# Performance work log

Hardware: AMD Instinct MI355X
Metric: run time of the kernel (lower is better)

The kernel has to match this reference:

```python
import jax, jax.numpy as jnp
import numpy as np

B, T, C, H = 65536, 100, 7, 2  # batch, timesteps, covariates, lstm hidden


def setup_inputs() -> dict:
    key = jax.random.key(0)
    ks = iter(jax.random.split(key, 32))
    def rn(shape, s=0.1):
        return jax.random.normal(next(ks), shape, dtype=jnp.float32) * s
    inp = {"x": jax.random.normal(next(ks), (B, T, C), dtype=jnp.float32)}
    for l, din in ((0, C), (1, 2 * H)):
        for suf in ("", "r"):
            inp[f"w_ih_l{l}{suf}"] = rn((4 * H, din))
            inp[f"w_hh_l{l}{suf}"] = rn((4 * H, H))
            inp[f"b_ih_l{l}{suf}"] = rn((4 * H,))
            inp[f"b_hh_l{l}{suf}"] = rn((4 * H,))
    inp["fc1_w"] = rn((64, 4 * T))
    inp["fc1_b"] = rn((64,))
    inp["fc2_w"] = rn((20, 64))
    inp["fc2_b"] = rn((20,))
    return inp


def _lstm_dir(xw, w_hh, b_hh, reverse):
    # xw: [T, B, 4H] precomputed input projection (x @ W_ih.T + b_ih)
    if reverse:
        xw = xw[::-1]
    h0 = jnp.zeros((xw.shape[1], H), xw.dtype)
    c0 = jnp.zeros((xw.shape[1], H), xw.dtype)

    def step(carry, gx):
        h, c = carry
        g = gx + h @ w_hh.T + b_hh            # [B, 4H]
        i, f, gg, o = jnp.split(g, 4, axis=-1)  # torch gate order i,f,g,o
        c = jax.nn.sigmoid(f) * c + jax.nn.sigmoid(i) * jnp.tanh(gg)
        h = jax.nn.sigmoid(o) * jnp.tanh(c)
        return (h, c), h

    _, hs = jax.lax.scan(step, (h0, c0), xw)
    if reverse:
        hs = hs[::-1]
    return hs  # [T, B, H]


def _bilstm_layer(x_tbf, w_ih_f, w_hh_f, b_ih_f, b_hh_f,
                  w_ih_b, w_hh_b, b_ih_b, b_hh_b):
    xw_f = jnp.einsum('tbc,gc->tbg', x_tbf, w_ih_f) + b_ih_f
    xw_b = jnp.einsum('tbc,gc->tbg', x_tbf, w_ih_b) + b_ih_b
    hf = _lstm_dir(xw_f, w_hh_f, b_hh_f, False)
    hb = _lstm_dir(xw_b, w_hh_b, b_hh_b, True)
    return jnp.concatenate([hf, hb], axis=-1)  # [T, B, 2H]


def reference(x,
              w_ih_l0, w_hh_l0, b_ih_l0, b_hh_l0,
              w_ih_l0r, w_hh_l0r, b_ih_l0r, b_hh_l0r,
              w_ih_l1, w_hh_l1, b_ih_l1, b_hh_l1,
              w_ih_l1r, w_hh_l1r, b_ih_l1r, b_hh_l1r,
              fc1_w, fc1_b, fc2_w, fc2_b):
    xt = jnp.transpose(x.reshape(-1, T, C), (1, 0, 2))  # [T, B, C] time-major
    h1 = _bilstm_layer(xt, w_ih_l0, w_hh_l0, b_ih_l0, b_hh_l0,
                       w_ih_l0r, w_hh_l0r, b_ih_l0r, b_hh_l0r)
    h2 = _bilstm_layer(h1, w_ih_l1, w_hh_l1, b_ih_l1, b_hh_l1,
                       w_ih_l1r, w_hh_l1r, b_ih_l1r, b_hh_l1r)
    out = jnp.transpose(h2, (1, 0, 2)).reshape(-1, 4 * T)  # flatten [B, 4T]
    out = jax.nn.relu(out)                  # relu BEFORE fc1, as in original
    out = jax.nn.relu(out @ fc1_w.T + fc1_b)
    return out @ fc2_w.T + fc2_b            # [B, 20]
```

## Files before the change

kernel.cpp:

```cpp
#include <hip/hip_runtime.h>

#define Bn 65536
#define Tn 100
#define Cn 7

typedef short short8 __attribute__((ext_vector_type(8)));
typedef float float4v __attribute__((ext_vector_type(4)));
typedef float float2v __attribute__((ext_vector_type(2)));

__device__ __forceinline__ float2v pk_fma(float2v a, float2v b, float2v c) {
    return __builtin_elementwise_fma(a, b, c);
}
__device__ __forceinline__ float2v pk2(float v) { return (float2v){v, v}; }

__device__ __forceinline__ float fast_rcp(float x) { return __builtin_amdgcn_rcpf(x); }
__device__ __forceinline__ float sig_f(float x) { return fast_rcp(1.f + __expf(-x)); }
__device__ __forceinline__ float tanh_f(float x) { return 1.f - 2.f * fast_rcp(__expf(2.f * x) + 1.f); }
__device__ __forceinline__ unsigned bf16rne(float x) {
    unsigned u = __float_as_uint(x);
    return (u + 0x7fffu + ((u >> 16) & 1u)) >> 16;
}
__device__ __forceinline__ float bf_lo(unsigned u) { return __uint_as_float(u << 16); }
__device__ __forceinline__ float bf_hi(unsigned u) { return __uint_as_float(u & 0xffff0000u); }

__device__ __forceinline__ float dpp_xor1(float x) {
    return __uint_as_float((unsigned)__builtin_amdgcn_mov_dpp(
        (int)__float_as_uint(x), 0xB1, 0xF, 0xF, true));
}

typedef const __attribute__((address_space(1))) void* gp_t;
typedef __attribute__((address_space(3))) void* sp_t;
__device__ __forceinline__ void async_copy_dw(const void* g, void* l) {
    __builtin_amdgcn_global_load_lds((gp_t)g, (sp_t)l, 4, 0, 0);
}

__global__ void w2prep_kernel(const float* __restrict__ fc1_w, unsigned short* __restrict__ w2g) {
    int idx = blockIdx.x * 256 + threadIdx.x;
    int w  = idx >> 12;
    int d  = (idx >> 11) & 1;
    int n  = (idx >> 5) & 63;
    int kk = idx & 31;
    int tt = kk >> 1, i = kk & 1;
    int t  = d ? (99 - 10 * w - tt) : (10 * w + tt);
    float v = (kk < 20) ? fc1_w[n * 400 + 4 * t + 2 * d + i] : 0.f;
    w2g[idx] = (unsigned short)bf16rne(v);
}

#define XFE(i) (xv[(i) >> 2][(i) & 3])
#define L0_STEP(RR, TV) do {                                                          \
    float2v g0 = bias2[0], g1 = bias2[1];                                             \
    g0 = pk_fma(wi2[0][0], pk2(XFE((RR)*7+0)), g0);                                   \
    g1 = pk_fma(wi2[1][0], pk2(XFE((RR)*7+0)), g1);                                   \
    g0 = pk_fma(wi2[0][1], pk2(XFE((RR)*7+1)), g0);                                   \
    g1 = pk_fma(wi2[1][1], pk2(XFE((RR)*7+1)), g1);                                   \
    g0 = pk_fma(wi2[0][2], pk2(XFE((RR)*7+2)), g0);                                   \
    g1 = pk_fma(wi2[1][2], pk2(XFE((RR)*7+2)), g1);                                   \
    g0 = pk_fma(wi2[0][3], pk2(XFE((RR)*7+3)), g0);                                   \
    g1 = pk_fma(wi2[1][3], pk2(XFE((RR)*7+3)), g1);                                   \
    g0 = pk_fma(wi2[0][4], pk2(XFE((RR)*7+4)), g0);                                   \
    g1 = pk_fma(wi2[1][4], pk2(XFE((RR)*7+4)), g1);                                   \
    g0 = pk_fma(wi2[0][5], pk2(XFE((RR)*7+5)), g0);                                   \
    g1 = pk_fma(wi2[1][5], pk2(XFE((RR)*7+5)), g1);                                   \
    g0 = pk_fma(wi2[0][6], pk2(XFE((RR)*7+6)), g0);                                   \
    g1 = pk_fma(wi2[1][6], pk2(XFE((RR)*7+6)), g1);                                   \
    g0 = pk_fma(whA2[0], pk2(hs), pk_fma(whB2[0], pk2(ho), g0));                      \
    g1 = pk_fma(whA2[1], pk2(hs), pk_fma(whB2[1], pk2(ho), g1));                      \
    const float iv = sig_f(g0.x);                                                     \
    const float fv = sig_f(g0.y);                                                     \
    const float qv = tanh_f(g1.x);                                                    \
    const float ov = sig_f(g1.y);                                                     \
    cc = fmaf(fv, cc, iv * qv);                                                       \
    hs = ov * tanh_f(cc);                                                             \
    ho = dpp_xor1(hs);                                                                \
    if (cid == 0)                                                                     \
        h1u[((size_t)(TV) * 2 + rev) * Bn + b] = bf16rne(hs) | (bf16rne(ho) << 16);   \
} while (0)

__global__ __launch_bounds__(256, 4) void l0_kernel(
    const float* __restrict__ x,
    const float* __restrict__ wih_f, const float* __restrict__ whh_f,
    const float* __restrict__ bih_f, const float* __restrict__ bhh_f,
    const float* __restrict__ wih_r, const float* __restrict__ whh_r,
    const float* __restrict__ bih_r, const float* __restrict__ bhh_r,
    unsigned* __restrict__ h1u)
{
    __shared__ float xs[4][2][896];

    const int tid  = threadIdx.x;
    const int wv   = tid >> 6;
    const int lane = tid & 63;
    const int rev  = wv >> 1;
    const int sgrp = wv & 1;
    const int cid  = lane & 1;
    const int s    = lane >> 1;
    const int b    = blockIdx.x * 64 + sgrp * 32 + s;

    const float* wih = rev ? wih_r : wih_f;
    const float* whh = rev ? whh_r : whh_f;
    const float* bih = rev ? bih_r : bih_f;
    const float* bhh = rev ? bhh_r : bhh_f;

    float2v wi2[2][7], whA2[2], whB2[2], bias2[2];
#pragma unroll
    for (int p = 0; p < 2; ++p) {
        const int k0 = cid + 4 * p, k1 = cid + 4 * p + 2;
#pragma unroll
        for (int c = 0; c < 7; ++c)
            wi2[p][c] = (float2v){wih[k0 * 7 + c], wih[k1 * 7 + c]};
        whA2[p]  = (float2v){whh[k0 * 2 + cid], whh[k1 * 2 + cid]};
        whB2[p]  = (float2v){whh[k0 * 2 + (cid ^ 1)], whh[k1 * 2 + (cid ^ 1)]};
        bias2[p] = (float2v){bih[k0] + bhh[k0], bih[k1] + bhh[k1]};
    }

    const int s0 = lane / 28;
    const int r0 = lane - 28 * s0;
    const float* xsamp = x + (size_t)(blockIdx.x * 64 + sgrp * 32 + s0) * 700;

    auto stage = [&](int ch, int p) {
        const int off = rev ? (672 - 28 * ch) : (28 * ch);
        const float* g = xsamp + off + r0;
        float* l = &xs[wv][p][lane];
        int r = r0;
#pragma unroll
        for (int i = 0; i < 14; ++i) {
            async_copy_dw(g, l);
            l += 64;
            const int c = (r >= 20) ? 1 : 0;
            g += c ? 2080 : 1408;
            r += c ? -20 : 8;
        }
    };

    float hs = 0.f, ho = 0.f, cc = 0.f;

    stage(0, 0);
#pragma unroll 1
    for (int chk = 0; chk < 25; ++chk) {
        if (chk == 0) __builtin_amdgcn_s_waitcnt(0x0F70);
        else          __builtin_amdgcn_s_waitcnt(0x0F74);
        __builtin_amdgcn_sched_barrier(0);
        if (chk < 24) stage(chk + 1, (chk + 1) & 1);
        __builtin_amdgcn_sched_barrier(0);

        const float* xp = &xs[wv][chk & 1][s * 28];
        float4v xv[7];
#pragma unroll
        for (int k = 0; k < 7; ++k) xv[k] = *(const float4v*)(xp + k * 4);

        if (rev) {
            const int t0 = 99 - 4 * chk;
            L0_STEP(3, t0);
            L0_STEP(2, t0 - 1);
            L0_STEP(1, t0 - 2);
            L0_STEP(0, t0 - 3);
        } else {
            const int t0 = 4 * chk;
            L0_STEP(0, t0);
            L0_STEP(1, t0 + 1);
            L0_STEP(2, t0 + 2);
            L0_STEP(3, t0 + 3);
        }
    }
}

__global__ __launch_bounds__(256, 4) void l1fc_kernel(
    const unsigned* __restrict__ hin,
    const float* __restrict__ wih_f, const float* __restrict__ whh_f,
    const float* __restrict__ bih_f, const float* __restrict__ bhh_f,
    const float* __restrict__ wih_r, const float* __restrict__ whh_r,
    const float* __restrict__ bih_r, const float* __restrict__ bhh_r,
    const unsigned* __restrict__ w2g,
    const float* __restrict__ fc1_b,
    const float* __restrict__ fc2_w,
    const float* __restrict__ fc2_b,
    float* __restrict__ out)
{
    __shared__ unsigned smem[7680];

    const int tid  = threadIdx.x;
    const int wv   = tid >> 6;
    const int lane = tid & 63;
    const int d    = wv >> 1;
    const int shalf = wv & 1;
    const int cid  = lane & 1;
    const int sp   = lane >> 1;
    const int b0   = blockIdx.x * 64;

    unsigned* a2w  = smem + wv * 640;
    unsigned* hstw = smem + 2560 + wv * 1280;

    const float* wih = d ? wih_r : wih_f;
    const float* whh = d ? whh_r : whh_f;
    const float* bih = d ? bih_r : bih_f;
    const float* bhh = d ? bhh_r : bhh_f;

    float2v wi2[2][4], whA2[2], whB2[2], bias2[2];
#pragma unroll
    for (int p = 0; p < 2; ++p) {
        const int k0 = cid + 4 * p, k1 = cid + 4 * p + 2;
#pragma unroll
        for (int m = 0; m < 4; ++m)
            wi2[p][m] = (float2v){wih[k0 * 4 + m], wih[k1 * 4 + m]};
        whA2[p]  = (float2v){whh[k0 * 2 + cid], whh[k1 * 2 + cid]};
        whB2[p]  = (float2v){whh[k0 * 2 + (cid ^ 1)], whh[k1 * 2 + (cid ^ 1)]};
        bias2[p] = (float2v){bih[k0] + bhh[k0], bih[k1] + bhh[k1]};
    }

    float4v acc[2][4];
#pragma unroll
    for (int mt = 0; mt < 2; ++mt)
#pragma unroll
        for (int nt = 0; nt < 4; ++nt) acc[mt][nt] = (float4v){0.f, 0.f, 0.f, 0.f};

    for (int i = lane; i < 640; i += 64) a2w[i] = 0u;

    auto stage_h = [&](int w, int pb) {
        unsigned* dst = hstw + pb * 640;
        const int col = lane & 31;
        const int Rb  = lane >> 5;
#pragma unroll
        for (int i = 0; i < 10; ++i) {
            const int R = Rb + 2 * i;
            const int p = (R >= 10) ? 1 : 0;
            const int j = R - 10 * p;
            const int t = d ? (99 - (10 * w + j)) : (10 * w + j);
            async_copy_dw(hin + ((size_t)t * 2 + p) * Bn + b0 + shalf * 32 + col,
                          dst + R * 32 + col);
        }
    };

    stage_h(0, 0);

    float hs = 0.f, ho = 0.f, cc = 0.f;
    const int q = lane >> 4, l16 = lane & 15;

#pragma unroll 1
    for (int w = 0; w < 10; ++w) {
        __builtin_amdgcn_s_waitcnt(0x0F70);
        __builtin_amdgcn_sched_barrier(0);

        short8 bv[4];
#pragma unroll
        for (int nt = 0; nt < 4; ++nt)
            bv[nt] = *(const short8*)&w2g[w * 2048 + d * 1024 + (nt * 16 + l16) * 16 + q * 4];

        if (w < 9) stage_h(w + 1, (w + 1) & 1);
        __builtin_amdgcn_sched_barrier(0);

        const unsigned* hb = hstw + (w & 1) * 640;
#pragma unroll 2
        for (int j = 0; j < 10; ++j) {
            const unsigned uF = hb[j * 32 + sp];
            const unsigned uR = hb[320 + j * 32 + sp];
            const float a0 = bf_lo(uF), a1 = bf_hi(uF);
            const float a2v = bf_lo(uR), a3 = bf_hi(uR);

            float2v g0 = bias2[0], g1 = bias2[1];
            g0 = pk_fma(wi2[0][0], pk2(a0), g0);  g1 = pk_fma(wi2[1][0], pk2(a0), g1);
            g0 = pk_fma(wi2[0][1], pk2(a1), g0);  g1 = pk_fma(wi2[1][1], pk2(a1), g1);
            g0 = pk_fma(wi2[0][2], pk2(a2v), g0); g1 = pk_fma(wi2[1][2], pk2(a2v), g1);
            g0 = pk_fma(wi2[0][3], pk2(a3), g0);  g1 = pk_fma(wi2[1][3], pk2(a3), g1);
            g0 = pk_fma(whA2[0], pk2(hs), pk_fma(whB2[0], pk2(ho), g0));
            g1 = pk_fma(whA2[1], pk2(hs), pk_fma(whB2[1], pk2(ho), g1));

            const float iv = sig_f(g0.x);
            const float fv = sig_f(g0.y);
            const float qv = tanh_f(g1.x);
            const float ov = sig_f(g1.y);
            cc = fmaf(fv, cc, iv * qv);
            hs = ov * tanh_f(cc);
            ho = dpp_xor1(hs);

            if (cid == 0)
                a2w[sp * 20 + j] = bf16rne(fmaxf(hs, 0.f)) | (bf16rne(fmaxf(ho, 0.f)) << 16);
        }
        asm volatile("s_waitcnt lgkmcnt(0)");
        __builtin_amdgcn_sched_barrier(0);

        {
            short8 av0 = *(const short8*)&a2w[l16 * 20 + q * 4];
            short8 av1 = *(const short8*)&a2w[(16 + l16) * 20 + q * 4];
#pragma unroll
            for (int nt = 0; nt < 4; ++nt) {
                acc[0][nt] = __builtin_amdgcn_mfma_f32_16x16x32_bf16(av0, bv[nt], acc[0][nt], 0, 0, 0);
                acc[1][nt] = __builtin_amdgcn_mfma_f32_16x16x32_bf16(av1, bv[nt], acc[1][nt], 0, 0, 0);
            }
        }
    }

    __syncthreads();
    float* eb = (float*)smem;
    if (d == 0) {
#pragma unroll
        for (int mt = 0; mt < 2; ++mt)
#pragma unroll
            for (int nt = 0; nt < 4; ++nt)
#pragma unroll
                for (int r = 0; r < 4; ++r)
                    eb[(shalf * 32 + mt * 16 + q * 4 + r) * 65 + nt * 16 + l16] = acc[mt][nt][r];
    }
    __syncthreads();
    if (d == 1) {
#pragma unroll
        for (int mt = 0; mt < 2; ++mt)
#pragma unroll
            for (int nt = 0; nt < 4; ++nt)
#pragma unroll
                for (int r = 0; r < 4; ++r)
                    eb[(shalf * 32 + mt * 16 + q * 4 + r) * 65 + nt * 16 + l16] += acc[mt][nt][r];
    }
    __syncthreads();

    const float* ebr = (const float*)smem;
    const int sm2 = tid & 63;
    const int og  = (tid >> 6) * 5;
    float z[64];
#pragma unroll
    for (int k = 0; k < 64; ++k) z[k] = fmaxf(ebr[sm2 * 65 + k] + fc1_b[k], 0.f);
    float y[5];
#pragma unroll
    for (int o = 0; o < 5; ++o) {
        float r2 = fc2_b[og + o];
#pragma unroll
        for (int k = 0; k < 64; ++k) r2 = fmaf(fc2_w[(og + o) * 64 + k], z[k], r2);
        y[o] = r2;
    }
    __syncthreads();
    float* ebw = (float*)smem;
#pragma unroll
    for (int o = 0; o < 5; ++o) ebw[sm2 * 20 + og + o] = y[o];
    __syncthreads();
    for (int f = tid; f < 1280; f += 256)
        out[(size_t)blockIdx.x * 1280 + f] = ebw[f];
}

extern "C" void kernel_launch(void* const* d_in, const int* in_sizes, int n_in,
                              void* d_out, int out_size, void* d_ws, size_t ws_size,
                              hipStream_t stream) {
    const float* x = (const float*)d_in[0];
    const float* w_ih_l0  = (const float*)d_in[1];
    const float* w_hh_l0  = (const float*)d_in[2];
    const float* b_ih_l0  = (const float*)d_in[3];
    const float* b_hh_l0  = (const float*)d_in[4];
    const float* w_ih_l0r = (const float*)d_in[5];
    const float* w_hh_l0r = (const float*)d_in[6];
    const float* b_ih_l0r = (const float*)d_in[7];
    const float* b_hh_l0r = (const float*)d_in[8];
    const float* w_ih_l1  = (const float*)d_in[9];
    const float* w_hh_l1  = (const float*)d_in[10];
    const float* b_ih_l1  = (const float*)d_in[11];
    const float* b_hh_l1  = (const float*)d_in[12];
    const float* w_ih_l1r = (const float*)d_in[13];
    const float* w_hh_l1r = (const float*)d_in[14];
    const float* b_ih_l1r = (const float*)d_in[15];
    const float* b_hh_l1r = (const float*)d_in[16];
    const float* fc1_w = (const float*)d_in[17];
    const float* fc1_b = (const float*)d_in[18];
    const float* fc2_w = (const float*)d_in[19];
    const float* fc2_b = (const float*)d_in[20];

    unsigned* h1u = (unsigned*)d_ws;
    unsigned short* w2g = (unsigned short*)((char*)d_ws + (size_t)Tn * 2 * Bn * 4);

    w2prep_kernel<<<160, 256, 0, stream>>>(fc1_w, w2g);
    l0_kernel<<<1024, 256, 0, stream>>>(x,
        w_ih_l0, w_hh_l0, b_ih_l0, b_hh_l0,
        w_ih_l0r, w_hh_l0r, b_ih_l0r, b_hh_l0r, h1u);
    l1fc_kernel<<<1024, 256, 0, stream>>>(h1u,
        w_ih_l1, w_hh_l1, b_ih_l1, b_hh_l1,
        w_ih_l1r, w_hh_l1r, b_ih_l1r, b_hh_l1r,
        (const unsigned*)w2g, fc1_b, fc2_w, fc2_b, (float*)d_out);
}
```

Measured before the change: 404.7 us.

## Split layer-0 LSTM gates across four lanes per sample instead of two

The layer-0 kernel now uses four lanes per (sample, direction) instead of two. Each lane computes one pair of gate pre-activations and one activation pair. Sigmoid and tanh share a single exp/rcp path selected by per-lane constants, and gates are exchanged with a DPP xor-2 swap. The grid doubles to 2048 blocks with 16 samples per wave, which halves the serial per-lane work on the recurrence's critical path. The cost is twice as many waves doing redundant x loads and cell-state updates, plus extra cross-lane moves.

```diff
diff --git a/kernel.cpp b/kernel.cpp
--- a/kernel.cpp
+++ b/kernel.cpp
@@ -26,6 +26,10 @@
 __device__ __forceinline__ float dpp_xor1(float x) {
     return __uint_as_float((unsigned)__builtin_amdgcn_mov_dpp(
         (int)__float_as_uint(x), 0xB1, 0xF, 0xF, true));
+}
+__device__ __forceinline__ float dpp_xor2(float x) {
+    return __uint_as_float((unsigned)__builtin_amdgcn_mov_dpp(
+        (int)__float_as_uint(x), 0x4E, 0xF, 0xF, true));
 }
 
 typedef const __attribute__((address_space(1))) void* gp_t;
@@ -48,32 +52,34 @@
 
 #define XFE(i) (xv[(i) >> 2][(i) & 3])
 #define L0_STEP(RR, TV) do {                                                          \
-    float2v g0 = bias2[0], g1 = bias2[1];                                             \
-    g0 = pk_fma(wi2[0][0], pk2(XFE((RR)*7+0)), g0);                                   \
-    g1 = pk_fma(wi2[1][0], pk2(XFE((RR)*7+0)), g1);                                   \
-    g0 = pk_fma(wi2[0][1], pk2(XFE((RR)*7+1)), g0);                                   \
-    g1 = pk_fma(wi2[1][1], pk2(XFE((RR)*7+1)), g1);                                   \
-    g0 = pk_fma(wi2[0][2], pk2(XFE((RR)*7+2)), g0);                                   \
-    g1 = pk_fma(wi2[1][2], pk2(XFE((RR)*7+2)), g1);                                   \
-    g0 = pk_fma(wi2[0][3], pk2(XFE((RR)*7+3)), g0);                                   \
-    g1 = pk_fma(wi2[1][3], pk2(XFE((RR)*7+3)), g1);                                   \
-    g0 = pk_fma(wi2[0][4], pk2(XFE((RR)*7+4)), g0);                                   \
-    g1 = pk_fma(wi2[1][4], pk2(XFE((RR)*7+4)), g1);                                   \
-    g0 = pk_fma(wi2[0][5], pk2(XFE((RR)*7+5)), g0);                                   \
-    g1 = pk_fma(wi2[1][5], pk2(XFE((RR)*7+5)), g1);                                   \
-    g0 = pk_fma(wi2[0][6], pk2(XFE((RR)*7+6)), g0);                                   \
-    g1 = pk_fma(wi2[1][6], pk2(XFE((RR)*7+6)), g1);                                   \
-    g0 = pk_fma(whA2[0], pk2(hs), pk_fma(whB2[0], pk2(ho), g0));                      \
-    g1 = pk_fma(whA2[1], pk2(hs), pk_fma(whB2[1], pk2(ho), g1));                      \
-    const float iv = sig_f(g0.x);                                                     \
-    const float fv = sig_f(g0.y);                                                     \
-    const float qv = tanh_f(g1.x);                                                    \
-    const float ov = sig_f(g1.y);                                                     \
-    cc = fmaf(fv, cc, iv * qv);                                                       \
-    hs = ov * tanh_f(cc);                                                             \
-    ho = dpp_xor1(hs);                                                                \
-    if (cid == 0)                                                                     \
-        h1u[((size_t)(TV) * 2 + rev) * Bn + b] = bf16rne(hs) | (bf16rne(ho) << 16);   \
+    float2v g = bias2;                                                                \
+    g = pk_fma(wi2[0], pk2(XFE((RR)*7+0)), g);                                        \
+    g = pk_fma(wi2[1], pk2(XFE((RR)*7+1)), g);                                        \
+    g = pk_fma(wi2[2], pk2(XFE((RR)*7+2)), g);                                        \
+    g = pk_fma(wi2[3], pk2(XFE((RR)*7+3)), g);                                        \
+    g = pk_fma(wi2[4], pk2(XFE((RR)*7+4)), g);                                        \
+    g = pk_fma(wi2[5], pk2(XFE((RR)*7+5)), g);                                        \
+    g = pk_fma(wi2[6], pk2(XFE((RR)*7+6)), g);                                        \
+    g = pk_fma(whX2, pk2(hA), pk_fma(whY2, pk2(hB), g));                              \
+    const float ex  = __expf(kx * g.x);                                               \
+    const float ey  = __expf(-g.y);                                                   \
+    const float rx  = fast_rcp(1.f + ex);                                             \
+    const float ry  = fast_rcp(1.f + ey);                                             \
+    const float acx = fmaf(ax_, rx, bx_);                                             \
+    const float acy = ry;                                                             \
+    const float swx = dpp_xor2(acx);                                                  \
+    const float swy = dpp_xor2(acy);                                                  \
+    const float iv  = qif ? acx : swx;                                                \
+    const float fv  = qif ? acy : swy;                                                \
+    const float gv  = qif ? swx : acx;                                                \
+    const float ov  = qif ? swy : acy;                                                \
+    cc = fmaf(fv, cc, iv * gv);                                                       \
+    const float th = tanh_f(cc);                                                      \
+    const float h  = ov * th;                                                         \
+    hB = dpp_xor1(h);                                                                 \
+    hA = h;                                                                           \
+    if (q == 0)                                                                       \
+        h1u[((size_t)(TV) * 2 + rev) * Bn + b] = bf16rne(hA) | (bf16rne(hB) << 16);   \
 } while (0)
 
 __global__ __launch_bounds__(256, 4) void l0_kernel(
@@ -84,45 +90,50 @@
     const float* __restrict__ bih_r, const float* __restrict__ bhh_r,
     unsigned* __restrict__ h1u)
 {
-    __shared__ float xs[4][2][896];
+    __shared__ float xs[4][2][448];
 
     const int tid  = threadIdx.x;
     const int wv   = tid >> 6;
     const int lane = tid & 63;
     const int rev  = wv >> 1;
     const int sgrp = wv & 1;
-    const int cid  = lane & 1;
-    const int s    = lane >> 1;
-    const int b    = blockIdx.x * 64 + sgrp * 32 + s;
+    const int sq   = lane >> 2;
+    const int q    = lane & 3;
+    const int ch   = q & 1;
+    const bool qif = (q & 2) == 0;
+    const int b    = blockIdx.x * 32 + sgrp * 16 + sq;
 
     const float* wih = rev ? wih_r : wih_f;
     const float* whh = rev ? whh_r : whh_f;
     const float* bih = rev ? bih_r : bih_f;
     const float* bhh = rev ? bhh_r : bhh_f;
 
-    float2v wi2[2][7], whA2[2], whB2[2], bias2[2];
-#pragma unroll
-    for (int p = 0; p < 2; ++p) {
-        const int k0 = cid + 4 * p, k1 = cid + 4 * p + 2;
-#pragma unroll
-        for (int c = 0; c < 7; ++c)
-            wi2[p][c] = (float2v){wih[k0 * 7 + c], wih[k1 * 7 + c]};
-        whA2[p]  = (float2v){whh[k0 * 2 + cid], whh[k1 * 2 + cid]};
-        whB2[p]  = (float2v){whh[k0 * 2 + (cid ^ 1)], whh[k1 * 2 + (cid ^ 1)]};
-        bias2[p] = (float2v){bih[k0] + bhh[k0], bih[k1] + bhh[k1]};
-    }
+    const int r0_ = (qif ? 0 : 4) + ch;
+    const int r1_ = (qif ? 2 : 6) + ch;
+
+    float2v wi2[7], whX2, whY2, bias2;
+#pragma unroll
+    for (int c = 0; c < 7; ++c)
+        wi2[c] = (float2v){wih[r0_ * 7 + c], wih[r1_ * 7 + c]};
+    whX2  = (float2v){whh[r0_ * 2 + ch], whh[r1_ * 2 + ch]};
+    whY2  = (float2v){whh[r0_ * 2 + (ch ^ 1)], whh[r1_ * 2 + (ch ^ 1)]};
+    bias2 = (float2v){bih[r0_] + bhh[r0_], bih[r1_] + bhh[r1_]};
+
+    const float kx  = qif ? -1.f : 2.f;
+    const float ax_ = qif ?  1.f : -2.f;
+    const float bx_ = qif ?  0.f : 1.f;
 
     const int s0 = lane / 28;
     const int r0 = lane - 28 * s0;
-    const float* xsamp = x + (size_t)(blockIdx.x * 64 + sgrp * 32 + s0) * 700;
-
-    auto stage = [&](int ch, int p) {
-        const int off = rev ? (672 - 28 * ch) : (28 * ch);
+    const float* xsamp = x + (size_t)(blockIdx.x * 32 + sgrp * 16 + s0) * 700;
+
+    auto stage = [&](int ch_, int p) {
+        const int off = rev ? (672 - 28 * ch_) : (28 * ch_);
         const float* g = xsamp + off + r0;
         float* l = &xs[wv][p][lane];
         int r = r0;
 #pragma unroll
-        for (int i = 0; i < 14; ++i) {
+        for (int i = 0; i < 7; ++i) {
             async_copy_dw(g, l);
             l += 64;
             const int c = (r >= 20) ? 1 : 0;
@@ -131,7 +142,7 @@
         }
     };
 
-    float hs = 0.f, ho = 0.f, cc = 0.f;
+    float hA = 0.f, hB = 0.f, cc = 0.f;
 
     stage(0, 0);
 #pragma unroll 1
@@ -142,7 +153,7 @@
         if (chk < 24) stage(chk + 1, (chk + 1) & 1);
         __builtin_amdgcn_sched_barrier(0);
 
-        const float* xp = &xs[wv][chk & 1][s * 28];
+        const float* xp = &xs[wv][chk & 1][sq * 28];
         float4v xv[7];
 #pragma unroll
         for (int k = 0; k < 7; ++k) xv[k] = *(const float4v*)(xp + k * 4);
@@ -363,7 +374,7 @@
     unsigned short* w2g = (unsigned short*)((char*)d_ws + (size_t)Tn * 2 * Bn * 4);
 
     w2prep_kernel<<<160, 256, 0, stream>>>(fc1_w, w2g);
-    l0_kernel<<<1024, 256, 0, stream>>>(x,
+    l0_kernel<<<2048, 256, 0, stream>>>(x,
         w_ih_l0, w_hh_l0, b_ih_l0, b_hh_l0,
         w_ih_l0r, w_hh_l0r, b_ih_l0r, b_hh_l0r, h1u);
     l1fc_kernel<<<1024, 256, 0, stream>>>(h1u,
```

Result: no change. 408.2 us (+0.9%).

## Fuse layer-0 and layer-1 LSTM kernels per block and prescale gates for exp2

Applied to the files above, without the earlier changes.

Merges the layer-0 BiLSTM kernel and the layer-1+FC kernel into one kernel. Each block computes its own 64 samples through both layers, with a vmcnt wait and block barrier between the phases, so the second launch and its tail are removed and h1 is likely re-read from L2. Gate weights and biases are premultiplied by log2(e) (or 2*log2(e) for the tanh gate) so activations use raw v_exp_f32 without an extra multiply. Launch bounds rise from 4 to 5 waves per SIMD, which may tighten register allocation. The fused kernel's footprint is the larger of the two phases.

```diff
diff --git a/kernel.cpp b/kernel.cpp
--- a/kernel.cpp
+++ b/kernel.cpp
@@ -3,6 +3,8 @@
 #define Bn 65536
 #define Tn 100
 #define Cn 7
+#define LOG2E  1.4426950408889634f
+#define LOG2E2 2.8853900817779268f
 
 typedef short short8 __attribute__((ext_vector_type(8)));
 typedef float float4v __attribute__((ext_vector_type(4)));
@@ -14,8 +16,12 @@
 __device__ __forceinline__ float2v pk2(float v) { return (float2v){v, v}; }
 
 __device__ __forceinline__ float fast_rcp(float x) { return __builtin_amdgcn_rcpf(x); }
-__device__ __forceinline__ float sig_f(float x) { return fast_rcp(1.f + __expf(-x)); }
-__device__ __forceinline__ float tanh_f(float x) { return 1.f - 2.f * fast_rcp(__expf(2.f * x) + 1.f); }
+__device__ __forceinline__ float exp2_f(float x) {
+    float r; asm("v_exp_f32 %0, %1" : "=v"(r) : "v"(x)); return r;
+}
+__device__ __forceinline__ float tanh2_f(float x) {
+    return 1.f - 2.f * fast_rcp(exp2_f(LOG2E2 * x) + 1.f);
+}
 __device__ __forceinline__ unsigned bf16rne(float x) {
     unsigned u = __float_as_uint(x);
     return (u + 0x7fffu + ((u >> 16) & 1u)) >> 16;
@@ -65,110 +71,28 @@
     g1 = pk_fma(wi2[1][6], pk2(XFE((RR)*7+6)), g1);                                   \
     g0 = pk_fma(whA2[0], pk2(hs), pk_fma(whB2[0], pk2(ho), g0));                      \
     g1 = pk_fma(whA2[1], pk2(hs), pk_fma(whB2[1], pk2(ho), g1));                      \
-    const float iv = sig_f(g0.x);                                                     \
-    const float fv = sig_f(g0.y);                                                     \
-    const float qv = tanh_f(g1.x);                                                    \
-    const float ov = sig_f(g1.y);                                                     \
+    const float iv = fast_rcp(1.f + exp2_f(-g0.x));                                   \
+    const float fv = fast_rcp(1.f + exp2_f(-g0.y));                                   \
+    const float qv = 1.f - 2.f * fast_rcp(exp2_f(g1.x) + 1.f);                        \
+    const float ov = fast_rcp(1.f + exp2_f(-g1.y));                                   \
     cc = fmaf(fv, cc, iv * qv);                                                       \
-    hs = ov * tanh_f(cc);                                                             \
+    hs = ov * tanh2_f(cc);                                                            \
     ho = dpp_xor1(hs);                                                                \
     if (cid == 0)                                                                     \
         h1u[((size_t)(TV) * 2 + rev) * Bn + b] = bf16rne(hs) | (bf16rne(ho) << 16);   \
 } while (0)
 
-__global__ __launch_bounds__(256, 4) void l0_kernel(
+__global__ __launch_bounds__(256, 5) void fused_kernel(
     const float* __restrict__ x,
-    const float* __restrict__ wih_f, const float* __restrict__ whh_f,
-    const float* __restrict__ bih_f, const float* __restrict__ bhh_f,
-    const float* __restrict__ wih_r, const float* __restrict__ whh_r,
-    const float* __restrict__ bih_r, const float* __restrict__ bhh_r,
-    unsigned* __restrict__ h1u)
-{
-    __shared__ float xs[4][2][896];
-
-    const int tid  = threadIdx.x;
-    const int wv   = tid >> 6;
-    const int lane = tid & 63;
-    const int rev  = wv >> 1;
-    const int sgrp = wv & 1;
-    const int cid  = lane & 1;
-    const int s    = lane >> 1;
-    const int b    = blockIdx.x * 64 + sgrp * 32 + s;
-
-    const float* wih = rev ? wih_r : wih_f;
-    const float* whh = rev ? whh_r : whh_f;
-    const float* bih = rev ? bih_r : bih_f;
-    const float* bhh = rev ? bhh_r : bhh_f;
-
-    float2v wi2[2][7], whA2[2], whB2[2], bias2[2];
-#pragma unroll
-    for (int p = 0; p < 2; ++p) {
-        const int k0 = cid + 4 * p, k1 = cid + 4 * p + 2;
-#pragma unroll
-        for (int c = 0; c < 7; ++c)
-            wi2[p][c] = (float2v){wih[k0 * 7 + c], wih[k1 * 7 + c]};
-        whA2[p]  = (float2v){whh[k0 * 2 + cid], whh[k1 * 2 + cid]};
-        whB2[p]  = (float2v){whh[k0 * 2 + (cid ^ 1)], whh[k1 * 2 + (cid ^ 1)]};
-        bias2[p] = (float2v){bih[k0] + bhh[k0], bih[k1] + bhh[k1]};
-    }
-
-    const int s0 = lane / 28;
-    const int r0 = lane - 28 * s0;
-    const float* xsamp = x + (size_t)(blockIdx.x * 64 + sgrp * 32 + s0) * 700;
-
-    auto stage = [&](int ch, int p) {
-        const int off = rev ? (672 - 28 * ch) : (28 * ch);
-        const float* g = xsamp + off + r0;
-        float* l = &xs[wv][p][lane];
-        int r = r0;
-#pragma unroll
-        for (int i = 0; i < 14; ++i) {
-            async_copy_dw(g, l);
-            l += 64;
-            const int c = (r >= 20) ? 1 : 0;
-            g += c ? 2080 : 1408;
-            r += c ? -20 : 8;
-        }
-    };
-
-    float hs = 0.f, ho = 0.f, cc = 0.f;
-
-    stage(0, 0);
-#pragma unroll 1
-    for (int chk = 0; chk < 25; ++chk) {
-        if (chk == 0) __builtin_amdgcn_s_waitcnt(0x0F70);
-        else          __builtin_amdgcn_s_waitcnt(0x0F74);
-        __builtin_amdgcn_sched_barrier(0);
-        if (chk < 24) stage(chk + 1, (chk + 1) & 1);
-        __builtin_amdgcn_sched_barrier(0);
-
-        const float* xp = &xs[wv][chk & 1][s * 28];
-        float4v xv[7];
-#pragma unroll
-        for (int k = 0; k < 7; ++k) xv[k] = *(const float4v*)(xp + k * 4);
-
-        if (rev) {
-            const int t0 = 99 - 4 * chk;
-            L0_STEP(3, t0);
-            L0_STEP(2, t0 - 1);
-            L0_STEP(1, t0 - 2);
-            L0_STEP(0, t0 - 3);
-        } else {
-            const int t0 = 4 * chk;
-            L0_STEP(0, t0);
-            L0_STEP(1, t0 + 1);
-            L0_STEP(2, t0 + 2);
-            L0_STEP(3, t0 + 3);
-        }
-    }
-}
-
-__global__ __launch_bounds__(256, 4) void l1fc_kernel(
-    const unsigned* __restrict__ hin,
-    const float* __restrict__ wih_f, const float* __restrict__ whh_f,
-    const float* __restrict__ bih_f, const float* __restrict__ bhh_f,
-    const float* __restrict__ wih_r, const float* __restrict__ whh_r,
-    const float* __restrict__ bih_r, const float* __restrict__ bhh_r,
+    const float* __restrict__ wih0_f, const float* __restrict__ whh0_f,
+    const float* __restrict__ bih0_f, const float* __restrict__ bhh0_f,
+    const float* __restrict__ wih0_r, const float* __restrict__ whh0_r,
+    const float* __restrict__ bih0_r, const float* __restrict__ bhh0_r,
+    unsigned* __restrict__ h1u,
+    const float* __restrict__ wih1_f, const float* __restrict__ whh1_f,
+    const float* __restrict__ bih1_f, const float* __restrict__ bhh1_f,
+    const float* __restrict__ wih1_r, const float* __restrict__ whh1_r,
+    const float* __restrict__ bih1_r, const float* __restrict__ bhh1_r,
     const unsigned* __restrict__ w2g,
     const float* __restrict__ fc1_b,
     const float* __restrict__ fc2_w,
@@ -180,158 +104,243 @@
     const int tid  = threadIdx.x;
     const int wv   = tid >> 6;
     const int lane = tid & 63;
-    const int d    = wv >> 1;
-    const int shalf = wv & 1;
-    const int cid  = lane & 1;
-    const int sp   = lane >> 1;
-    const int b0   = blockIdx.x * 64;
-
-    unsigned* a2w  = smem + wv * 640;
-    unsigned* hstw = smem + 2560 + wv * 1280;
-
-    const float* wih = d ? wih_r : wih_f;
-    const float* whh = d ? whh_r : whh_f;
-    const float* bih = d ? bih_r : bih_f;
-    const float* bhh = d ? bhh_r : bhh_f;
-
-    float2v wi2[2][4], whA2[2], whB2[2], bias2[2];
-#pragma unroll
-    for (int p = 0; p < 2; ++p) {
-        const int k0 = cid + 4 * p, k1 = cid + 4 * p + 2;
-#pragma unroll
-        for (int m = 0; m < 4; ++m)
-            wi2[p][m] = (float2v){wih[k0 * 4 + m], wih[k1 * 4 + m]};
-        whA2[p]  = (float2v){whh[k0 * 2 + cid], whh[k1 * 2 + cid]};
-        whB2[p]  = (float2v){whh[k0 * 2 + (cid ^ 1)], whh[k1 * 2 + (cid ^ 1)]};
-        bias2[p] = (float2v){bih[k0] + bhh[k0], bih[k1] + bhh[k1]};
+
+    {
+        float* xs = (float*)smem;
+        const int rev  = wv >> 1;
+        const int sgrp = wv & 1;
+        const int cid  = lane & 1;
+        const int s    = lane >> 1;
+        const int b    = blockIdx.x * 64 + sgrp * 32 + s;
+
+        const float* wih = rev ? wih0_r : wih0_f;
+        const float* whh = rev ? whh0_r : whh0_f;
+        const float* bih = rev ? bih0_r : bih0_f;
+        const float* bhh = rev ? bhh0_r : bhh0_f;
+
+        const float2v sc[2] = { (float2v){LOG2E, LOG2E}, (float2v){LOG2E2, LOG2E} };
+        float2v wi2[2][7], whA2[2], whB2[2], bias2[2];
+#pragma unroll
+        for (int p = 0; p < 2; ++p) {
+            const int k0 = cid + 4 * p, k1 = cid + 4 * p + 2;
+#pragma unroll
+            for (int c = 0; c < 7; ++c)
+                wi2[p][c] = (float2v){wih[k0 * 7 + c], wih[k1 * 7 + c]} * sc[p];
+            whA2[p]  = (float2v){whh[k0 * 2 + cid], whh[k1 * 2 + cid]} * sc[p];
+            whB2[p]  = (float2v){whh[k0 * 2 + (cid ^ 1)], whh[k1 * 2 + (cid ^ 1)]} * sc[p];
+            bias2[p] = (float2v){bih[k0] + bhh[k0], bih[k1] + bhh[k1]} * sc[p];
+        }
+
+        const int s0 = lane / 28;
+        const int r0 = lane - 28 * s0;
+        const float* xsamp = x + (size_t)(blockIdx.x * 64 + sgrp * 32 + s0) * 700;
+
+        auto stage = [&](int ch, int p) {
+            const int off = rev ? (672 - 28 * ch) : (28 * ch);
+            const float* g = xsamp + off + r0;
+            float* l = xs + wv * 1792 + p * 896 + lane;
+            int r = r0;
+#pragma unroll
+            for (int i = 0; i < 14; ++i) {
+                async_copy_dw(g, l);
+                l += 64;
+                const int c = (r >= 20) ? 1 : 0;
+                g += c ? 2080 : 1408;
+                r += c ? -20 : 8;
+            }
+        };
+
+        float hs = 0.f, ho = 0.f, cc = 0.f;
+
+        stage(0, 0);
+#pragma unroll 1
+        for (int chk = 0; chk < 25; ++chk) {
+            if (chk == 0) __builtin_amdgcn_s_waitcnt(0x0F70);
+            else          __builtin_amdgcn_s_waitcnt(0x0F74);
+            __builtin_amdgcn_sched_barrier(0);
+            if (chk < 24) stage(chk + 1, (chk + 1) & 1);
+            __builtin_amdgcn_sched_barrier(0);
+
+            const float* xp = xs + wv * 1792 + (chk & 1) * 896 + s * 28;
+            float4v xv[7];
+#pragma unroll
+            for (int k = 0; k < 7; ++k) xv[k] = *(const float4v*)(xp + k * 4);
+
+            if (rev) {
+                const int t0 = 99 - 4 * chk;
+                L0_STEP(3, t0);
+                L0_STEP(2, t0 - 1);
+                L0_STEP(1, t0 - 2);
+                L0_STEP(0, t0 - 3);
+            } else {
+                const int t0 = 4 * chk;
+                L0_STEP(0, t0);
+                L0_STEP(1, t0 + 1);
+                L0_STEP(2, t0 + 2);
+                L0_STEP(3, t0 + 3);
+            }
+        }
     }
 
-    float4v acc[2][4];
-#pragma unroll
-    for (int mt = 0; mt < 2; ++mt)
-#pragma unroll
-        for (int nt = 0; nt < 4; ++nt) acc[mt][nt] = (float4v){0.f, 0.f, 0.f, 0.f};
-
-    for (int i = lane; i < 640; i += 64) a2w[i] = 0u;
-
-    auto stage_h = [&](int w, int pb) {
-        unsigned* dst = hstw + pb * 640;
-        const int col = lane & 31;
-        const int Rb  = lane >> 5;
-#pragma unroll
-        for (int i = 0; i < 10; ++i) {
-            const int R = Rb + 2 * i;
-            const int p = (R >= 10) ? 1 : 0;
-            const int j = R - 10 * p;
-            const int t = d ? (99 - (10 * w + j)) : (10 * w + j);
-            async_copy_dw(hin + ((size_t)t * 2 + p) * Bn + b0 + shalf * 32 + col,
-                          dst + R * 32 + col);
-        }
-    };
-
-    stage_h(0, 0);
-
-    float hs = 0.f, ho = 0.f, cc = 0.f;
-    const int q = lane >> 4, l16 = lane & 15;
+    asm volatile("s_waitcnt vmcnt(0)");
+    __syncthreads();
+
+    {
+        const unsigned* hin = (const unsigned*)h1u;
+        const int d     = wv >> 1;
+        const int shalf = wv & 1;
+        const int cid   = lane & 1;
+        const int sp    = lane >> 1;
+        const int b0    = blockIdx.x * 64;
+
+        unsigned* a2w  = smem + wv * 640;
+        unsigned* hstw = smem + 2560 + wv * 1280;
+
+        const float* wih = d ? wih1_r : wih1_f;
+        const float* whh = d ? whh1_r : whh1_f;
+        const float* bih = d ? bih1_r : bih1_f;
+        const float* bhh = d ? bhh1_r : bhh1_f;
+
+        const float2v sc[2] = { (float2v){LOG2E, LOG2E}, (float2v){LOG2E2, LOG2E} };
+        float2v wi2[2][4], whA2[2], whB2[2], bias2[2];
+#pragma unroll
+        for (int p = 0; p < 2; ++p) {
+            const int k0 = cid + 4 * p, k1 = cid + 4 * p + 2;
+#pragma unroll
+            for (int m = 0; m < 4; ++m)
+                wi2[p][m] = (float2v){wih[k0 * 4 + m], wih[k1 * 4 + m]} * sc[p];
+            whA2[p]  = (float2v){whh[k0 * 2 + cid], whh[k1 * 2 + cid]} * sc[p];
+            whB2[p]  = (float2v){whh[k0 * 2 + (cid ^ 1)], whh[k1 * 2 + (cid ^ 1)]} * sc[p];
+            bias2[p] = (float2v){bih[k0] + bhh[k0], bih[k1] + bhh[k1]} * sc[p];
+        }
+
+        float4v acc[2][4];
+#pragma unroll
+        for (int mt = 0; mt < 2; ++mt)
+#pragma unroll
+            for (int nt = 0; nt < 4; ++nt) acc[mt][nt] = (float4v){0.f, 0.f, 0.f, 0.f};
+
+        for (int i = lane; i < 640; i += 64) a2w[i] = 0u;
+
+        auto stage_h = [&](int w, int pb) {
+            unsigned* dst = hstw + pb * 640;
+            const int col = lane & 31;
+            const int Rb  = lane >> 5;
+#pragma unroll
+            for (int i = 0; i < 10; ++i) {
+                const int R = Rb + 2 * i;
+                const int p = (R >= 10) ? 1 : 0;
+                const int j = R - 10 * p;
+                const int t = d ? (99 - (10 * w + j)) : (10 * w + j);
+                async_copy_dw(hin + ((size_t)t * 2 + p) * Bn + b0 + shalf * 32 + col,
+                              dst + R * 32 + col);
+            }
+        };
+
+        stage_h(0, 0);
+
+        float hs = 0.f, ho = 0.f, cc = 0.f;
+        const int q = lane >> 4, l16 = lane & 15;
 
 #pragma unroll 1
-    for (int w = 0; w < 10; ++w) {
-        __builtin_amdgcn_s_waitcnt(0x0F70);
-        __builtin_amdgcn_sched_barrier(0);
-
-        short8 bv[4];
-#pragma unroll
-        for (int nt = 0; nt < 4; ++nt)
-            bv[nt] = *(const short8*)&w2g[w * 2048 + d * 1024 + (nt * 16 + l16) * 16 + q * 4];
-
-        if (w < 9) stage_h(w + 1, (w + 1) & 1);
-        __builtin_amdgcn_sched_barrier(0);
-
-        const unsigned* hb = hstw + (w & 1) * 640;
+        for (int w = 0; w < 10; ++w) {
+            __builtin_amdgcn_s_waitcnt(0x0F70);
+            __builtin_amdgcn_sched_barrier(0);
+
+            short8 bv[4];
+#pragma unroll
+            for (int nt = 0; nt < 4; ++nt)
+                bv[nt] = *(const short8*)&w2g[w * 2048 + d * 1024 + (nt * 16 + l16) * 16 + q * 4];
+
+            if (w < 9) stage_h(w + 1, (w + 1) & 1);
+            __builtin_amdgcn_sched_barrier(0);
+
+            const unsigned* hb = hstw + (w & 1) * 640;
 #pragma unroll 2
-        for (int j = 0; j < 10; ++j) {
-            const unsigned uF = hb[j * 32 + sp];
-            const unsigned uR = hb[320 + j * 32 + sp];
-            const float a0 = bf_lo(uF), a1 = bf_hi(uF);
-            const float a2v = bf_lo(uR), a3 = bf_hi(uR);
-
-            float2v g0 = bias2[0], g1 = bias2[1];
-            g0 = pk_fma(wi2[0][0], pk2(a0), g0);  g1 = pk_fma(wi2[1][0], pk2(a0), g1);
-            g0 = pk_fma(wi2[0][1], pk2(a1), g0);  g1 = pk_fma(wi2[1][1], pk2(a1), g1);
-            g0 = pk_fma(wi2[0][2], pk2(a2v), g0); g1 = pk_fma(wi2[1][2], pk2(a2v), g1);
-            g0 = pk_fma(wi2[0][3], pk2(a3), g0);  g1 = pk_fma(wi2[1][3], pk2(a3), g1);
-            g0 = pk_fma(whA2[0], pk2(hs), pk_fma(whB2[0], pk2(ho), g0));
-            g1 = pk_fma(whA2[1], pk2(hs), pk_fma(whB2[1], pk2(ho), g1));
-
-            const float iv = sig_f(g0.x);
-            const float fv = sig_f(g0.y);
-            const float qv = tanh_f(g1.x);
-            const float ov = sig_f(g1.y);
-            cc = fmaf(fv, cc, iv * qv);
-            hs = ov * tanh_f(cc);
-            ho = dpp_xor1(hs);
-
-            if (cid == 0)
-                a2w[sp * 20 + j] = bf16rne(fmaxf(hs, 0.f)) | (bf16rne(fmaxf(ho, 0.f)) << 16);
-        }
-        asm volatile("s_waitcnt lgkmcnt(0)");
-        __builtin_amdgcn_sched_barrier(0);
-
-        {
-            short8 av0 = *(const short8*)&a2w[l16 * 20 + q * 4];
-            short8 av1 = *(const short8*)&a2w[(16 + l16) * 20 + q * 4];
-#pragma unroll
-            for (int nt = 0; nt < 4; ++nt) {
-                acc[0][nt] = __builtin_amdgcn_mfma_f32_16x16x32_bf16(av0, bv[nt], acc[0][nt], 0, 0, 0);
-                acc[1][nt] = __builtin_amdgcn_mfma_f32_16x16x32_bf16(av1, bv[nt], acc[1][nt], 0, 0, 0);
-            }
-        }
+            for (int j = 0; j < 10; ++j) {
+                const unsigned uF = hb[j * 32 + sp];
+                const unsigned uR = hb[320 + j * 32 + sp];
+                const float a0 = bf_lo(uF), a1 = bf_hi(uF);
+                const float a2v = bf_lo(uR), a3 = bf_hi(uR);
+
+                float2v g0 = bias2[0], g1 = bias2[1];
+                g0 = pk_fma(wi2[0][0], pk2(a0), g0);  g1 = pk_fma(wi2[1][0], pk2(a0), g1);
+                g0 = pk_fma(wi2[0][1], pk2(a1), g0);  g1 = pk_fma(wi2[1][1], pk2(a1), g1);
+                g0 = pk_fma(wi2[0][2], pk2(a2v), g0); g1 = pk_fma(wi2[1][2], pk2(a2v), g1);
+                g0 = pk_fma(wi2[0][3], pk2(a3), g0);  g1 = pk_fma(wi2[1][3], pk2(a3), g1);
+                g0 = pk_fma(whA2[0], pk2(hs), pk_fma(whB2[0], pk2(ho), g0));
+                g1 = pk_fma(whA2[1], pk2(hs), pk_fma(whB2[1], pk2(ho), g1));
+
+                const float iv = fast_rcp(1.f + exp2_f(-g0.x));
+                const float fv = fast_rcp(1.f + exp2_f(-g0.y));
+                const float qv = 1.f - 2.f * fast_rcp(exp2_f(g1.x) + 1.f);
+                const float ov = fast_rcp(1.f + exp2_f(-g1.y));
+                cc = fmaf(fv, cc, iv * qv);
+                hs = ov * tanh2_f(cc);
+                ho = dpp_xor1(hs);
+
+                if (cid == 0)
+                    a2w[sp * 20 + j] = bf16rne(fmaxf(hs, 0.f)) | (bf16rne(fmaxf(ho, 0.f)) << 16);
+            }
+            asm volatile("s_waitcnt lgkmcnt(0)");
+            __builtin_amdgcn_sched_barrier(0);
+
+            {
+                short8 av0 = *(const short8*)&a2w[l16 * 20 + q * 4];
+                short8 av1 = *(const short8*)&a2w[(16 + l16) * 20 + q * 4];
+#pragma unroll
+                for (int nt = 0; nt < 4; ++nt) {
+                    acc[0][nt] = __builtin_amdgcn_mfma_f32_16x16x32_bf16(av0, bv[nt], acc[0][nt], 0, 0, 0);
+                    acc[1][nt] = __builtin_amdgcn_mfma_f32_16x16x32_bf16(av1, bv[nt], acc[1][nt], 0, 0, 0);
+                }
+            }
+        }
+
+        __syncthreads();
+        float* eb = (float*)smem;
+        if (d == 0) {
+#pragma unroll
+            for (int mt = 0; mt < 2; ++mt)
+#pragma unroll
+                for (int nt = 0; nt < 4; ++nt)
+#pragma unroll
+                    for (int r = 0; r < 4; ++r)
+                        eb[(shalf * 32 + mt * 16 + q * 4 + r) * 65 + nt * 16 + l16] = acc[mt][nt][r];
+        }
+        __syncthreads();
+        if (d == 1) {
+#pragma unroll
+            for (int mt = 0; mt < 2; ++mt)
+#pragma unroll
+                for (int nt = 0; nt < 4; ++nt)
+#pragma unroll
+                    for (int r = 0; r < 4; ++r)
+                        eb[(shalf * 32 + mt * 16 + q * 4 + r) * 65 + nt * 16 + l16] += acc[mt][nt][r];
+        }
+        __syncthreads();
+
+        const float* ebr = (const float*)smem;
+        const int sm2 = tid & 63;
+        const int og  = (tid >> 6) * 5;
+        float z[64];
+#pragma unroll
+        for (int k = 0; k < 64; ++k) z[k] = fmaxf(ebr[sm2 * 65 + k] + fc1_b[k], 0.f);
+        float y[5];
+#pragma unroll
+        for (int o = 0; o < 5; ++o) {
+            float r2 = fc2_b[og + o];
+#pragma unroll
+            for (int k = 0; k < 64; ++k) r2 = fmaf(fc2_w[(og + o) * 64 + k], z[k], r2);
+            y[o] = r2;
+        }
+        __syncthreads();
+        float* ebw = (float*)smem;
+#pragma unroll
+        for (int o = 0; o < 5; ++o) ebw[sm2 * 20 + og + o] = y[o];
+        __syncthreads();
+        for (int f = tid; f < 1280; f += 256)
+            out[(size_t)blockIdx.x * 1280 + f] = ebw[f];
     }
-
-    __syncthreads();
-    float* eb = (float*)smem;
-    if (d == 0) {
-#pragma unroll
-        for (int mt = 0; mt < 2; ++mt)
-#pragma unroll
-            for (int nt = 0; nt < 4; ++nt)
-#pragma unroll
-                for (int r = 0; r < 4; ++r)
-                    eb[(shalf * 32 + mt * 16 + q * 4 + r) * 65 + nt * 16 + l16] = acc[mt][nt][r];
-    }
-    __syncthreads();
-    if (d == 1) {
-#pragma unroll
-        for (int mt = 0; mt < 2; ++mt)
-#pragma unroll
-            for (int nt = 0; nt < 4; ++nt)
-#pragma unroll
-                for (int r = 0; r < 4; ++r)
-                    eb[(shalf * 32 + mt * 16 + q * 4 + r) * 65 + nt * 16 + l16] += acc[mt][nt][r];
-    }
-    __syncthreads();
-
-    const float* ebr = (const float*)smem;
-    const int sm2 = tid & 63;
-    const int og  = (tid >> 6) * 5;
-    float z[64];
-#pragma unroll
-    for (int k = 0; k < 64; ++k) z[k] = fmaxf(ebr[sm2 * 65 + k] + fc1_b[k], 0.f);
-    float y[5];
-#pragma unroll
-    for (int o = 0; o < 5; ++o) {
-        float r2 = fc2_b[og + o];
-#pragma unroll
-        for (int k = 0; k < 64; ++k) r2 = fmaf(fc2_w[(og + o) * 64 + k], z[k], r2);
-        y[o] = r2;
-    }
-    __syncthreads();
-    float* ebw = (float*)smem;
-#pragma unroll
-    for (int o = 0; o < 5; ++o) ebw[sm2 * 20 + og + o] = y[o];
-    __syncthreads();
-    for (int f = tid; f < 1280; f += 256)
-        out[(size_t)blockIdx.x * 1280 + f] = ebw[f];
 }
 
 extern "C" void kernel_launch(void* const* d_in, const int* in_sizes, int n_in,
@@ -363,10 +372,9 @@
     unsigned short* w2g = (unsigned short*)((char*)d_ws + (size_t)Tn * 2 * Bn * 4);
 
     w2prep_kernel<<<160, 256, 0, stream>>>(fc1_w, w2g);
-    l0_kernel<<<1024, 256, 0, stream>>>(x,
+    fused_kernel<<<1024, 256, 0, stream>>>(x,
         w_ih_l0, w_hh_l0, b_ih_l0, b_hh_l0,
-        w_ih_l0r, w_hh_l0r, b_ih_l0r, b_hh_l0r, h1u);
-    l1fc_kernel<<<1024, 256, 0, stream>>>(h1u,
+        w_ih_l0r, w_hh_l0r, b_ih_l0r, b_hh_l0r, h1u,
         w_ih_l1, w_hh_l1, b_ih_l1, b_hh_l1,
         w_ih_l1r, w_hh_l1r, b_ih_l1r, b_hh_l1r,
         (const unsigned*)w2g, fc1_b, fc2_w, fc2_b, (float*)d_out);
```

New measurement: 570.1 us. 1.41x slower.
